# Kernel tuning notes

Measured on AMD Instinct MI355X. Metric: run time of the kernel, lower is better.

The kernel has to match this reference:

```python
import jax, jax.numpy as jnp
import numpy as np

NPOINT = 2048
RADII = (0.4, 0.8)
NSAMPLES = (16, 32)
EPS = 1e-5


def _fps(xyz, npoint):
    # iterative farthest point sampling, start at index 0 (matches CUDA kernel)
    B, N, _ = xyz.shape

    def step(carry, _):
        dist, last = carry  # dist [B,N], last [B]
        lx = jnp.take_along_axis(xyz, last[:, None, None], axis=1)  # [B,1,3]
        d = jnp.sum((xyz - lx) ** 2, axis=-1)  # [B,N]
        dist = jnp.minimum(dist, d)
        nxt = jnp.argmax(dist, axis=1).astype(jnp.int32)
        return (dist, nxt), last

    init = (jnp.full((B, N), 1e10, xyz.dtype), jnp.zeros((B,), jnp.int32))
    _, idxs = jax.lax.scan(step, init, None, length=npoint)
    return idxs.T  # [B, npoint]


def _ball_query(radius, nsample, xyz, new_xyz):
    # first-nsample points within radius, in original order; pad with first hit (0 if none)
    N = xyz.shape[1]
    d2 = jnp.sum((new_xyz[:, :, None, :] - xyz[:, None, :, :]) ** 2, axis=-1)  # [B,S,N]
    mask = d2 < radius * radius
    ar = jnp.arange(N, dtype=jnp.int32)
    key = jnp.where(mask, ar, N + ar)  # in-range first, stable original order
    order = jnp.argsort(key, axis=-1)[..., :nsample].astype(jnp.int32)  # [B,S,ns]
    cnt = mask.sum(axis=-1, keepdims=True)  # [B,S,1]
    valid = jnp.arange(nsample) < cnt
    return jnp.where(valid, order, order[..., :1])


def _bn_relu(x):
    # training-mode BatchNorm (gamma=1, beta=0) over all dims but channel (last)
    red = tuple(range(x.ndim - 1))
    mu = x.mean(axis=red, keepdims=True)
    var = x.var(axis=red, keepdims=True)
    return jax.nn.relu((x - mu) * jax.lax.rsqrt(var + EPS))


def _scale(xyz, new_xyz, feats, radius, nsample, ws):
    idx = _ball_query(radius, nsample, xyz, new_xyz)  # [B,S,ns]
    B, S, ns = idx.shape
    flat = idx.reshape(B, S * ns)
    gx = jnp.take_along_axis(xyz, flat[..., None], axis=1).reshape(B, S, ns, 3)
    gx = gx - new_xyz[:, :, None, :]  # relative coords
    gf = jnp.take_along_axis(feats, flat[..., None], axis=1).reshape(B, S, ns, -1)
    h = jnp.concatenate([gx, gf], axis=-1)  # [B,S,ns,3+C]
    for w in ws:
        h = _bn_relu(h @ w)  # pointwise conv (kernel 1) + BN + ReLU
    return h.max(axis=2)  # max-pool over group -> [B,S,Cout]


def setup_inputs() -> dict:
    key = jax.random.key(0)
    ks = jax.random.split(key, 16)
    s = 0.02
    return {
        "xyz": jax.random.normal(ks[0], (8, 8192, 3), jnp.float32),
        "features": jax.random.normal(ks[1], (8, 8192, 64), jnp.float32),
        "w0_0": jax.random.normal(ks[2], (67, 64), jnp.float32) * s,
        "w0_1": jax.random.normal(ks[3], (64, 64), jnp.float32) * s,
        "w0_2": jax.random.normal(ks[4], (64, 128), jnp.float32) * s,
        "w1_0": jax.random.normal(ks[5], (67, 64), jnp.float32) * s,
        "w1_1": jax.random.normal(ks[6], (64, 64), jnp.float32) * s,
        "w1_2": jax.random.normal(ks[7], (64, 128), jnp.float32) * s,
        "agg_w": jax.random.normal(ks[8], (256, 256), jnp.float32) * s,
        "agg_b": jax.random.normal(ks[9], (256,), jnp.float32) * s,
        "conf_w": jax.random.normal(ks[10], (256, 256), jnp.float32) * s,
        "cls_w": jax.random.normal(ks[11], (256, 3), jnp.float32) * s,
        "cls_b": jax.random.normal(ks[12], (3,), jnp.float32) * s,
    }


def reference(xyz, features, w0_0, w0_1, w0_2, w1_0, w1_1, w1_2,
              agg_w, agg_b, conf_w, cls_w, cls_b):
    idx = _fps(xyz, NPOINT)  # [B,S]
    new_xyz = jnp.take_along_axis(xyz, idx[..., None], axis=1)  # [B,S,3]
    f0 = _scale(xyz, new_xyz, features, RADII[0], NSAMPLES[0], (w0_0, w0_1, w0_2))
    f1 = _scale(xyz, new_xyz, features, RADII[1], NSAMPLES[1], (w1_0, w1_1, w1_2))
    h = jnp.concatenate([f0, f1], axis=-1)  # [B,S,256]
    h = _bn_relu(h @ agg_w + agg_b)  # aggregation Linear + BN + ReLU
    c = _bn_relu(h @ conf_w)  # confidence hidden layer
    cls = c @ cls_w + cls_b  # [B,S,num_class]
    return new_xyz, h, cls
```

## Files before the change

kernel.cpp:

```cpp
#include <hip/hip_runtime.h>
#include <cstdint>
#include <cstddef>

constexpr int Bb = 8;
constexpr int Nn = 8192;
constexpr int Ss = 2048;
constexpr int BS = Bb * Ss;
constexpr int NSL = 32;

typedef float vfloat2 __attribute__((ext_vector_type(2)));

__global__ __launch_bounds__(1024) void fps_kernel(const float* __restrict__ xyz,
                                                   float* __restrict__ new_xyz) {
  __shared__ float lx[Nn * 3];
  __shared__ int sidx[Ss];
  __shared__ unsigned long long slotV[2];
  __shared__ int slotI[2];
  const int b = blockIdx.x;
  const int tid = threadIdx.x;
  const float* xb = xyz + (size_t)b * Nn * 3;
  for (int e = tid; e < Nn * 3; e += 1024) lx[e] = xb[e];
  if (tid == 0) {
    slotV[0] = 0ull; slotV[1] = 0ull;
    slotI[0] = 0x7fffffff; slotI[1] = 0x7fffffff;
  }
  __syncthreads();

  vfloat2 px2[4], py2[4], pz2[4], df2[4];
  double dist[8];
#pragma unroll
  for (int jj = 0; jj < 4; ++jj) {
    const int p0 = tid + (2 * jj) * 1024, p1 = tid + (2 * jj + 1) * 1024;
    px2[jj] = (vfloat2){lx[p0 * 3 + 0], lx[p1 * 3 + 0]};
    py2[jj] = (vfloat2){lx[p0 * 3 + 1], lx[p1 * 3 + 1]};
    pz2[jj] = (vfloat2){lx[p0 * 3 + 2], lx[p1 * 3 + 2]};
    df2[jj] = (vfloat2){3.0e38f, 3.0e38f};
    dist[2 * jj] = 1e10;
    dist[2 * jj + 1] = 1e10;
  }
  float lmax = 3.0e38f;
  int cur = 0;
  double lv = -1.0;
  int li = 0x7fffffff;
  float lv32 = -1.0f;
  float wv32_c = -1.0f;
  for (int i = 0; i < Ss; ++i) {
    if (tid == 0) sidx[i] = cur;
    const float cxf = lx[cur * 3 + 0], cyf = lx[cur * 3 + 1], czf = lx[cur * 3 + 2];
    const vfloat2 cx2 = {cxf, cxf}, cy2 = {cyf, cyf}, cz2 = {czf, czf};
    const bool wasTop = (lv32 == wv32_c);
    vfloat2 d2v[4];
#pragma unroll
    for (int jj = 0; jj < 4; ++jj) {
      const vfloat2 dx = px2[jj] - cx2;
      const vfloat2 dy = py2[jj] - cy2;
      const vfloat2 dz = pz2[jj] - cz2;
      d2v[jj] = dx * dx + dy * dy + dz * dz;
    }
    const float dmin = fminf(fminf(fminf(d2v[0].x, d2v[0].y), fminf(d2v[1].x, d2v[1].y)),
                             fminf(fminf(d2v[2].x, d2v[2].y), fminf(d2v[3].x, d2v[3].y)));
    bool changed = false;
    if (dmin <= lmax) {
#pragma unroll
      for (int j = 0; j < 8; ++j) {
        const float d2s = d2v[j >> 1][j & 1];
        const float dfs = (j & 1) ? df2[j >> 1].y : df2[j >> 1].x;
        if (d2s <= dfs) {
          const float pxs = px2[j >> 1][j & 1];
          const float pys = py2[j >> 1][j & 1];
          const float pzs = pz2[j >> 1][j & 1];
          double dx = __dsub_rn((double)pxs, (double)cxf);
          double dy = __dsub_rn((double)pys, (double)cyf);
          double dz = __dsub_rn((double)pzs, (double)czf);
          double d = __dadd_rn(__dadd_rn(__dmul_rn(dx, dx), __dmul_rn(dy, dy)),
                               __dmul_rn(dz, dz));
          if (d < dist[j]) {
            dist[j] = d;
            const float dfn = (float)d * 1.000002f;
            if (j & 1) df2[j >> 1].y = dfn; else df2[j >> 1].x = dfn;
            changed = true;
          }
        }
      }
      if (changed) {
        lv = -1.0;
        li = 0;
#pragma unroll
        for (int j = 0; j < 8; ++j) {
          if (dist[j] > lv) { lv = dist[j]; li = tid + j * 1024; }
        }
        lv32 = (float)lv;
        lmax = fmaxf(fmaxf(fmaxf(df2[0].x, df2[0].y), fmaxf(df2[1].x, df2[1].y)),
                     fmaxf(fmaxf(df2[2].x, df2[2].y), fmaxf(df2[3].x, df2[3].y)));
      }
    }
    const unsigned long long topChanged = __ballot(changed && wasTop);
    if (topChanged) {
      float m32 = lv32;
#pragma unroll
      for (int off = 1; off < 64; off <<= 1) m32 = fmaxf(m32, __shfl_xor(m32, off));
      wv32_c = m32;
    }
    const int pb = i & 1;
    if (lv32 == wv32_c) atomicMax(&slotV[pb], (unsigned long long)__double_as_longlong(lv));
    __syncthreads();
    const double W = __longlong_as_double((long long)slotV[pb]);
    if (lv == W) atomicMin(&slotI[pb], li);
    if (tid == 0) {
      slotV[pb ^ 1] = 0ull;
      slotI[pb ^ 1] = 0x7fffffff;
    }
    __syncthreads();
    cur = slotI[pb];
  }
  __syncthreads();
  float* nxb = new_xyz + (size_t)b * Ss * 3;
  for (int e = tid; e < Ss * 3; e += 1024) {
    const int i = e / 3, c = e - i * 3;
    nxb[e] = lx[sidx[i] * 3 + c];
  }
}

__global__ __launch_bounds__(256) void ballq_kernel(const float* __restrict__ xyz,
                                                    const float* __restrict__ nxyz,
                                                    int* __restrict__ idx0,
                                                    int* __restrict__ idx1) {
  const int wid = threadIdx.x >> 6, lane = threadIdx.x & 63;
  const int bs = blockIdx.x * 4 + wid;
  const int b = bs >> 11;
  const float* xb = xyz + (size_t)b * Nn * 3;
  const float cxf = nxyz[bs * 3 + 0];
  const float cyf = nxyz[bs * 3 + 1];
  const float czf = nxyz[bs * 3 + 2];
  const double R0d = 0.4 * 0.4, R1d = 0.8 * 0.8;
  const float R0lo = 0.16f * (1.0f - 1e-5f), R0hi = 0.16f * (1.0f + 1e-5f);
  const float R1lo = 0.64f * (1.0f - 1e-5f), R1hi = 0.64f * (1.0f + 1e-5f);
  int cnt0 = 0, cnt1 = 0, first0 = 0, first1 = 0;
  const unsigned long long lmask = (1ull << lane) - 1ull;
  for (int base = 0; base < Nn; base += 64) {
    const int p = base + lane;
    const float pxs = xb[p * 3 + 0], pys = xb[p * 3 + 1], pzs = xb[p * 3 + 2];
    const float dxf = pxs - cxf, dyf = pys - cyf, dzf = pzs - czf;
    const float d2f = fmaf(dxf, dxf, fmaf(dyf, dyf, dzf * dzf));
    bool in0, in1;
    if (d2f < R0lo) in0 = true;
    else if (d2f > R0hi) in0 = false;
    else {
      double dx = __dsub_rn((double)pxs, (double)cxf);
      double dy = __dsub_rn((double)pys, (double)cyf);
      double dz = __dsub_rn((double)pzs, (double)czf);
      double d2 = __dadd_rn(__dadd_rn(__dmul_rn(dx, dx), __dmul_rn(dy, dy)), __dmul_rn(dz, dz));
      in0 = d2 < R0d;
    }
    if (d2f < R1lo) in1 = true;
    else if (d2f > R1hi) in1 = false;
    else {
      double dx = __dsub_rn((double)pxs, (double)cxf);
      double dy = __dsub_rn((double)pys, (double)cyf);
      double dz = __dsub_rn((double)pzs, (double)czf);
      double d2 = __dadd_rn(__dadd_rn(__dmul_rn(dx, dx), __dmul_rn(dy, dy)), __dmul_rn(dz, dz));
      in1 = d2 < R1d;
    }
    unsigned long long m0 = __ballot(in0);
    unsigned long long m1 = __ballot(in1);
    if (cnt0 < 16 && m0) {
      if (cnt0 == 0) first0 = base + __builtin_ctzll(m0);
      int r = (int)__popcll(m0 & lmask);
      if (in0 && cnt0 + r < 16) idx0[bs * 16 + cnt0 + r] = p;
      cnt0 += (int)__popcll(m0);
    }
    if (cnt1 < 32 && m1) {
      if (cnt1 == 0) first1 = base + __builtin_ctzll(m1);
      int r = (int)__popcll(m1 & lmask);
      if (in1 && cnt1 + r < 32) idx1[bs * 32 + cnt1 + r] = p;
      cnt1 += (int)__popcll(m1);
    }
    if (cnt0 >= 16 && cnt1 >= 32) break;
  }
  const int f0 = cnt0 < 16 ? cnt0 : 16;
  for (int j = f0 + lane; j < 16; j += 64) idx0[bs * 16 + j] = first0;
  const int f1 = cnt1 < 32 ? cnt1 : 32;
  for (int j = f1 + lane; j < 32; j += 64) idx1[bs * 32 + j] = first1;
}

template <int COUT, int KTOT, int MODE, int NS, bool POOL, bool BIAS>
__global__ __launch_bounds__(256) void mlp_gemm(
    const float* __restrict__ xin, const float* __restrict__ xin2,
    const float* __restrict__ stIn, const float* __restrict__ stIn2,
    float invM1, float invM2,
    const float* __restrict__ w, const float* __restrict__ bias,
    const int* __restrict__ gidx, const float* __restrict__ xyz,
    const float* __restrict__ nxyz, const float* __restrict__ feats,
    float* __restrict__ hw, float* __restrict__ out, float* __restrict__ Sout) {
  constexpr int KC = (KTOT <= 68) ? KTOT : 32;
  constexpr int NCH = (KTOT + KC - 1) / KC;
  constexpr int TC = COUT / 16;
  constexpr int TC2 = TC / 2;
  constexpr int XPAD = KC + 1;
  constexpr int XSZ = 64 * XPAD;
  constexpr int EPI = (POOL ? 48 : 32) * COUT;
  constexpr int SM = (XSZ + KC * COUT > EPI) ? (XSZ + KC * COUT) : EPI;
  constexpr int BNSZ = (MODE == 0) ? 0 : 512;
  __shared__ float smem[SM + BNSZ];
  __shared__ int rowP[(MODE == 0) ? 64 : 1];
  __shared__ float rowC[(MODE == 0) ? 192 : 1];
  float* xS = smem;
  float* wS = smem + XSZ;
  float* bnM = smem + SM;
  float* bnR = smem + SM + 256;

  const int tid = threadIdx.x;
  const int cg = tid & 15, rg = tid >> 4;
  const int row0 = blockIdx.x * 64;

  if constexpr (MODE == 0) {
    if (tid < 64) {
      const int rowg = row0 + tid;
      const int bs = rowg / NS;
      const int bb = bs >> 11;
      rowP[tid] = bb * Nn + gidx[rowg];
      rowC[tid * 3 + 0] = nxyz[bs * 3 + 0];
      rowC[tid * 3 + 1] = nxyz[bs * 3 + 1];
      rowC[tid * 3 + 2] = nxyz[bs * 3 + 2];
    }
    __syncthreads();
  } else {
    for (int c = tid; c < KTOT; c += 256) {
      float sum = 0.f, sq = 0.f, im;
      if constexpr (MODE == 2) {
        const float* base = (c < 128) ? stIn : stIn2;
        const int cc = (c < 128) ? c : c - 128;
        im = (c < 128) ? invM1 : invM2;
#pragma unroll
        for (int s = 0; s < NSL; ++s) {
          sum += base[cc * NSL + s];
          sq += base[(128 + cc) * NSL + s];
        }
      } else {
        constexpr int C = (MODE == 1) ? 64 : 256;
        im = invM1;
#pragma unroll
        for (int s = 0; s < NSL; ++s) {
          sum += stIn[c * NSL + s];
          sq += stIn[(C + c) * NSL + s];
        }
      }
      const float mu = sum * im;
      const float var = sq * im - mu * mu;
      bnM[c] = mu;
      bnR[c] = 1.0f / sqrtf(var + 1e-5f);
    }
    __syncthreads();
  }

  vfloat2 acc2[4][TC2];
#pragma unroll
  for (int i = 0; i < 4; ++i)
#pragma unroll
    for (int t = 0; t < TC2; ++t) acc2[i][t] = (vfloat2){0.f, 0.f};

  for (int ch = 0; ch < NCH; ++ch) {
    const int k0 = ch * KC;
    if (ch) __syncthreads();
    for (int e = tid; e < 64 * KC; e += 256) {
      const int r = e / KC, kk = e - r * KC;
      const int kg = k0 + kk;
      const int rowg = row0 + r;
      float v;
      if constexpr (MODE == 0) {
        if (kg < 3)
          v = xyz[rowP[r] * 3 + kg] - rowC[r * 3 + kg];
        else
          v = feats[(rowP[r] << 6) + (kg - 3)];
      } else if constexpr (MODE == 1) {
        v = fmaxf((xin[(size_t)rowg * 64 + kg] - bnM[kg]) * bnR[kg], 0.f);
      } else if constexpr (MODE == 2) {
        if (kg < 128)
          v = fmaxf((xin[(size_t)rowg * 128 + kg] - bnM[kg]) * bnR[kg], 0.f);
        else
          v = fmaxf((xin2[(size_t)rowg * 128 + (kg - 128)] - bnM[kg]) * bnR[kg], 0.f);
      } else {
        v = fmaxf((xin[(size_t)rowg * 256 + kg] - bnM[kg]) * bnR[kg], 0.f);
        hw[(size_t)rowg * 256 + kg] = v;
      }
      xS[r * XPAD + kk] = v;
    }
    for (int e = tid; e < KC * COUT; e += 256) {
      const int kk = e / COUT, c = e - kk * COUT;
      wS[kk * COUT + c] = w[(size_t)(k0 + kk) * COUT + c];
    }
    __syncthreads();
    for (int kk = 0; kk < KC; ++kk) {
      vfloat2 x2[4];
#pragma unroll
      for (int i = 0; i < 4; ++i) {
        const float xr = xS[(rg * 4 + i) * XPAD + kk];
        x2[i] = (vfloat2){xr, xr};
      }
#pragma unroll
      for (int t2 = 0; t2 < TC2; t2 += 2) {
        const float4 wv = *(const float4*)&wS[kk * COUT + cg * TC + 2 * t2];
        const vfloat2 w0 = {wv.x, wv.y}, w1 = {wv.z, wv.w};
#pragma unroll
        for (int i = 0; i < 4; ++i) {
          acc2[i][t2] += x2[i] * w0;
          acc2[i][t2 + 1] += x2[i] * w1;
        }
      }
    }
  }
  __syncthreads();
  if constexpr (BIAS) {
#pragma unroll
    for (int t = 0; t < TC; ++t) {
      const float bv = bias[cg * TC + t];
#pragma unroll
      for (int i = 0; i < 4; ++i) {
        if (t & 1) acc2[i][t >> 1].y += bv; else acc2[i][t >> 1].x += bv;
      }
    }
  }
  float* ssum = smem;
  float* ssq = smem + 16 * COUT;
  float* pbuf = smem + 32 * COUT;
  const int colb = cg * TC;
#pragma unroll
  for (int t = 0; t < TC; ++t) {
    float s = 0.f, q = 0.f, m = -3.4e38f;
#pragma unroll
    for (int i = 0; i < 4; ++i) {
      const float v = (t & 1) ? acc2[i][t >> 1].y : acc2[i][t >> 1].x;
      s += v;
      q = fmaf(v, v, q);
      m = fmaxf(m, v);
    }
    ssum[rg * COUT + colb + t] = s;
    ssq[rg * COUT + colb + t] = q;
    if constexpr (POOL) pbuf[rg * COUT + colb + t] = m;
  }
  __syncthreads();
  const int slot = blockIdx.x & (NSL - 1);
  for (int c = tid; c < COUT; c += 256) {
    float s = 0.f, q = 0.f;
#pragma unroll
    for (int rr = 0; rr < 16; ++rr) {
      s += ssum[rr * COUT + c];
      q += ssq[rr * COUT + c];
    }
    atomicAdd(&Sout[c * NSL + slot], s);
    atomicAdd(&Sout[(COUT + c) * NSL + slot], q);
  }
  if constexpr (POOL) {
    constexpr int G = 64 / NS, RPG = NS / 4;
    for (int o = tid; o < G * COUT; o += 256) {
      const int g = o / COUT, c = o - g * COUT;
      float m = pbuf[(g * RPG) * COUT + c];
#pragma unroll
      for (int qq = 1; qq < RPG; ++qq) m = fmaxf(m, pbuf[(g * RPG + qq) * COUT + c]);
      out[(size_t)(blockIdx.x * G + g) * COUT + c] = m;
    }
  } else {
#pragma unroll
    for (int i = 0; i < 4; ++i) {
      float* op = out + (size_t)(row0 + rg * 4 + i) * COUT + colb;
#pragma unroll
      for (int t2 = 0; t2 < TC2; t2 += 2) {
        *(float4*)(op + 2 * t2) = make_float4(acc2[i][t2].x, acc2[i][t2].y,
                                              acc2[i][t2 + 1].x, acc2[i][t2 + 1].y);
      }
    }
  }
}

__global__ __launch_bounds__(256) void cls_kernel(const float* __restrict__ craw,
                                                  const float* __restrict__ st,
                                                  const float* __restrict__ clsw,
                                                  const float* __restrict__ clsb,
                                                  float* __restrict__ outc) {
  __shared__ float bnM[256], bnR[256];
  const int tid = threadIdx.x;
  {
    float sum = 0.f, sq = 0.f;
#pragma unroll
    for (int s = 0; s < NSL; ++s) {
      sum += st[tid * NSL + s];
      sq += st[(256 + tid) * NSL + s];
    }
    const float im = 1.0f / 16384.0f;
    const float mu = sum * im;
    const float var = sq * im - mu * mu;
    bnM[tid] = mu;
    bnR[tid] = 1.0f / sqrtf(var + 1e-5f);
  }
  __syncthreads();
  const int wid = tid >> 6, lane = tid & 63;
  const int row = blockIdx.x * 4 + wid;
  const float* cr = craw + (size_t)row * 256;
  float a0 = 0.f, a1 = 0.f, a2 = 0.f;
#pragma unroll 4
  for (int k = lane; k < 256; k += 64) {
    float x = fmaxf((cr[k] - bnM[k]) * bnR[k], 0.f);
    a0 = fmaf(x, clsw[k * 3 + 0], a0);
    a1 = fmaf(x, clsw[k * 3 + 1], a1);
    a2 = fmaf(x, clsw[k * 3 + 2], a2);
  }
#pragma unroll
  for (int off = 32; off; off >>= 1) {
    a0 += __shfl_down(a0, off);
    a1 += __shfl_down(a1, off);
    a2 += __shfl_down(a2, off);
  }
  if (lane == 0) {
    outc[row * 3 + 0] = a0 + clsb[0];
    outc[row * 3 + 1] = a1 + clsb[1];
    outc[row * 3 + 2] = a2 + clsb[2];
  }
}

extern "C" void kernel_launch(void* const* d_in, const int* in_sizes, int n_in,
                              void* d_out, int out_size, void* d_ws, size_t ws_size,
                              hipStream_t stream) {
  (void)in_sizes; (void)n_in; (void)out_size; (void)ws_size;
  const float* xyz = (const float*)d_in[0];
  const float* feats = (const float*)d_in[1];
  const float* w00 = (const float*)d_in[2];
  const float* w01 = (const float*)d_in[3];
  const float* w02 = (const float*)d_in[4];
  const float* w10 = (const float*)d_in[5];
  const float* w11 = (const float*)d_in[6];
  const float* w12 = (const float*)d_in[7];
  const float* aggw = (const float*)d_in[8];
  const float* aggb = (const float*)d_in[9];
  const float* confw = (const float*)d_in[10];
  const float* clsw = (const float*)d_in[11];
  const float* clsb = (const float*)d_in[12];

  float* outp = (float*)d_out;
  float* nxyz = outp;
  float* hout = outp + (size_t)BS * 3;
  float* clsout = hout + (size_t)BS * 256;

  char* ws = (char*)d_ws;
  const size_t MB = 1u << 20;
  int* idx0 = (int*)(ws + 0);
  int* idx1 = (int*)(ws + 1 * MB);
  float* st = (float*)(ws + 3 * MB);
  float* pool0 = (float*)(ws + 12 * MB);
  float* pool1 = (float*)(ws + 20 * MB);
  float* aggraw = (float*)(ws + 28 * MB);
  float* confraw = (float*)(ws + 44 * MB);
  float* hA = (float*)(ws + 60 * MB);

  hipMemsetAsync(st, 0, 65536 * sizeof(float), stream);

  const float iM0 = 1.0f / 262144.0f;
  const float iM1 = 1.0f / 524288.0f;
  const float iMh = 1.0f / 16384.0f;

  fps_kernel<<<Bb, 1024, 0, stream>>>(xyz, nxyz);
  ballq_kernel<<<BS / 4, 256, 0, stream>>>(xyz, nxyz, idx0, idx1);

  mlp_gemm<64, 67, 0, 16, false, false><<<4096, 256, 0, stream>>>(
      nullptr, nullptr, nullptr, nullptr, 0.f, 0.f, w00, nullptr,
      idx0, xyz, nxyz, feats, nullptr, hA, st + 0);
  mlp_gemm<64, 64, 1, 1, false, false><<<4096, 256, 0, stream>>>(
      hA, nullptr, st + 0, nullptr, iM0, 0.f, w01, nullptr,
      nullptr, nullptr, nullptr, nullptr, nullptr, hA, st + 4096);
  mlp_gemm<128, 64, 1, 16, true, false><<<4096, 256, 0, stream>>>(
      hA, nullptr, st + 4096, nullptr, iM0, 0.f, w02, nullptr,
      nullptr, nullptr, nullptr, nullptr, nullptr, pool0, st + 8192);

  mlp_gemm<64, 67, 0, 32, false, false><<<8192, 256, 0, stream>>>(
      nullptr, nullptr, nullptr, nullptr, 0.f, 0.f, w10, nullptr,
      idx1, xyz, nxyz, feats, nullptr, hA, st + 16384);
  mlp_gemm<64, 64, 1, 1, false, false><<<8192, 256, 0, stream>>>(
      hA, nullptr, st + 16384, nullptr, iM1, 0.f, w11, nullptr,
      nullptr, nullptr, nullptr, nullptr, nullptr, hA, st + 20480);
  mlp_gemm<128, 64, 1, 32, true, false><<<8192, 256, 0, stream>>>(
      hA, nullptr, st + 20480, nullptr, iM1, 0.f, w12, nullptr,
      nullptr, nullptr, nullptr, nullptr, nullptr, pool1, st + 24576);

  mlp_gemm<256, 256, 2, 1, false, true><<<256, 256, 0, stream>>>(
      pool0, pool1, st + 8192, st + 24576, iM0, iM1, aggw, aggb,
      nullptr, nullptr, nullptr, nullptr, nullptr, aggraw, st + 32768);

  mlp_gemm<256, 256, 4, 1, false, false><<<256, 256, 0, stream>>>(
      aggraw, nullptr, st + 32768, nullptr, iMh, 0.f, confw, nullptr,
      nullptr, nullptr, nullptr, nullptr, hout, confraw, st + 49152);

  cls_kernel<<<BS / 4, 256, 0, stream>>>(confraw, st + 49152, clsw, clsb, clsout);
}
```

Measured before the change: 3.679 ms.

## Replace FPS shared-memory atomics with per-wave argmax and cross-wave shuffle reduction

Swaps the two-phase atomicMax/atomicMin argmax in farthest point sampling for a cached per-wave (value, index) winner in double precision. The winner is recomputed by shuffles only when the top lane changed, written per wave to a double-buffered shared array, and reduced across the 16 waves by every wave with shuffles. This removes one __syncthreads per iteration and the shared atomics. In exchange each wave does a redundant 16-entry reduction with 64-bit shuffles, and the cached per-wave reduction uses doubles instead of floats.

Result: slower. 4.714 ms (+28.1%).

```diff
diff --git a/kernel.cpp b/kernel.cpp
--- a/kernel.cpp
+++ b/kernel.cpp
@@ -14,16 +14,13 @@
                                                    float* __restrict__ new_xyz) {
   __shared__ float lx[Nn * 3];
   __shared__ int sidx[Ss];
-  __shared__ unsigned long long slotV[2];
-  __shared__ int slotI[2];
+  __shared__ double sVal[2][16];
+  __shared__ int sIdxW[2][16];
   const int b = blockIdx.x;
   const int tid = threadIdx.x;
+  const int wid = tid >> 6, lane = tid & 63;
   const float* xb = xyz + (size_t)b * Nn * 3;
   for (int e = tid; e < Nn * 3; e += 1024) lx[e] = xb[e];
-  if (tid == 0) {
-    slotV[0] = 0ull; slotV[1] = 0ull;
-    slotI[0] = 0x7fffffff; slotI[1] = 0x7fffffff;
-  }
   __syncthreads();
 
   vfloat2 px2[4], py2[4], pz2[4], df2[4];
@@ -42,13 +39,13 @@
   int cur = 0;
   double lv = -1.0;
   int li = 0x7fffffff;
-  float lv32 = -1.0f;
-  float wv32_c = -1.0f;
+  double wVal = -1.0;
+  int wIdx = 0x7fffffff;
   for (int i = 0; i < Ss; ++i) {
     if (tid == 0) sidx[i] = cur;
     const float cxf = lx[cur * 3 + 0], cyf = lx[cur * 3 + 1], czf = lx[cur * 3 + 2];
     const vfloat2 cx2 = {cxf, cxf}, cy2 = {cyf, cyf}, cz2 = {czf, czf};
-    const bool wasTop = (lv32 == wv32_c);
+    const bool wasTop = (lv == wVal);
     vfloat2 d2v[4];
 #pragma unroll
     for (int jj = 0; jj < 4; ++jj) {
@@ -89,29 +86,37 @@
         for (int j = 0; j < 8; ++j) {
           if (dist[j] > lv) { lv = dist[j]; li = tid + j * 1024; }
         }
-        lv32 = (float)lv;
         lmax = fmaxf(fmaxf(fmaxf(df2[0].x, df2[0].y), fmaxf(df2[1].x, df2[1].y)),
                      fmaxf(fmaxf(df2[2].x, df2[2].y), fmaxf(df2[3].x, df2[3].y)));
       }
     }
-    const unsigned long long topChanged = __ballot(changed && wasTop);
-    if (topChanged) {
-      float m32 = lv32;
-#pragma unroll
-      for (int off = 1; off < 64; off <<= 1) m32 = fmaxf(m32, __shfl_xor(m32, off));
-      wv32_c = m32;
+    if (__any(changed && wasTop)) {
+      double v = lv;
+      int ii = li;
+#pragma unroll
+      for (int off = 1; off < 64; off <<= 1) {
+        const double ov = __shfl_xor(v, off);
+        const int oi = __shfl_xor(ii, off);
+        if (ov > v || (ov == v && oi < ii)) { v = ov; ii = oi; }
+      }
+      wVal = v;
+      wIdx = ii;
     }
     const int pb = i & 1;
-    if (lv32 == wv32_c) atomicMax(&slotV[pb], (unsigned long long)__double_as_longlong(lv));
+    if (lane == 0) {
+      sVal[pb][wid] = wVal;
+      sIdxW[pb][wid] = wIdx;
+    }
     __syncthreads();
-    const double W = __longlong_as_double((long long)slotV[pb]);
-    if (lv == W) atomicMin(&slotI[pb], li);
-    if (tid == 0) {
-      slotV[pb ^ 1] = 0ull;
-      slotI[pb ^ 1] = 0x7fffffff;
-    }
-    __syncthreads();
-    cur = slotI[pb];
+    double bv = sVal[pb][lane & 15];
+    int bi = sIdxW[pb][lane & 15];
+#pragma unroll
+    for (int off = 1; off < 16; off <<= 1) {
+      const double ov = __shfl_xor(bv, off);
+      const int oi = __shfl_xor(bi, off);
+      if (ov > bv || (ov == bv && oi < bi)) { bv = ov; bi = oi; }
+    }
+    cur = bi;
   }
   __syncthreads();
   float* nxb = new_xyz + (size_t)b * Ss * 3;
```

## Run pointwise MLP GEMMs on MFMA using split-bf16 three-product emulation

Applied to the files above, without the earlier changes.

Replaces the scalar FP32 register-tiled GEMM in mlp_gemm with bf16 MFMA 16x16x32 instructions. Each operand is split into high and low bf16 parts, and three products are accumulated to approximate FP32 precision. K is padded to a multiple of 32, weights are stored transposed in LDS, and the epilogue is remapped to the MFMA output layout. The GEMM FLOPs move onto matrix cores, at the cost of extra conversion work and an approximation of full FP32 accuracy. The total time likely includes FPS and ball query, which this change leaves untouched.

Result: no change. 3.725 ms (+1.3%).

```diff
diff --git a/kernel.cpp b/kernel.cpp
--- a/kernel.cpp
+++ b/kernel.cpp
@@ -9,6 +9,13 @@
 constexpr int NSL = 32;
 
 typedef float vfloat2 __attribute__((ext_vector_type(2)));
+typedef short bf16x8 __attribute__((ext_vector_type(8)));
+typedef float f32x4 __attribute__((ext_vector_type(4)));
+
+__device__ __forceinline__ unsigned short f32_to_bf16(float f) {
+  unsigned u = __float_as_uint(f);
+  return (unsigned short)((u + 0x7FFFu + ((u >> 16) & 1u)) >> 16);
+}
 
 __global__ __launch_bounds__(1024) void fps_kernel(const float* __restrict__ xyz,
                                                    float* __restrict__ new_xyz) {
@@ -192,25 +199,31 @@
     const int* __restrict__ gidx, const float* __restrict__ xyz,
     const float* __restrict__ nxyz, const float* __restrict__ feats,
     float* __restrict__ hw, float* __restrict__ out, float* __restrict__ Sout) {
-  constexpr int KC = (KTOT <= 68) ? KTOT : 32;
-  constexpr int NCH = (KTOT + KC - 1) / KC;
-  constexpr int TC = COUT / 16;
-  constexpr int TC2 = TC / 2;
-  constexpr int XPAD = KC + 1;
-  constexpr int XSZ = 64 * XPAD;
-  constexpr int EPI = (POOL ? 48 : 32) * COUT;
-  constexpr int SM = (XSZ + KC * COUT > EPI) ? (XSZ + KC * COUT) : EPI;
-  constexpr int BNSZ = (MODE == 0) ? 0 : 512;
-  __shared__ float smem[SM + BNSZ];
+  constexpr int KP = (KTOT + 31) & ~31;
+  constexpr int KC = (KP <= 96) ? KP : 64;
+  constexpr int NCH = KP / KC;
+  constexpr int CT = COUT / 16;
+  constexpr int XPus = KC + 8;
+  constexpr int XPL = 64 * XPus;
+  constexpr int WPL = COUT * XPus;
+  constexpr size_t STAGE_B = (size_t)(2 * XPL + 2 * WPL) * 2;
+  constexpr size_t EPI_B = (size_t)(POOL ? 48 : 32) * COUT * 4;
+  constexpr size_t BODY_B = (STAGE_B > EPI_B) ? STAGE_B : EPI_B;
+  constexpr size_t BN_B = (MODE == 0) ? 0 : 2048;
+  __shared__ __align__(16) unsigned char smraw[BODY_B + BN_B];
   __shared__ int rowP[(MODE == 0) ? 64 : 1];
   __shared__ float rowC[(MODE == 0) ? 192 : 1];
-  float* xS = smem;
-  float* wS = smem + XSZ;
-  float* bnM = smem + SM;
-  float* bnR = smem + SM + 256;
+  unsigned short* xH = (unsigned short*)smraw;
+  unsigned short* xL = xH + XPL;
+  unsigned short* wH = xL + XPL;
+  unsigned short* wL = wH + WPL;
+  float* bnM = (float*)(smraw + BODY_B);
+  float* bnR = bnM + 256;
 
   const int tid = threadIdx.x;
-  const int cg = tid & 15, rg = tid >> 4;
+  const int l15 = tid & 15;
+  const int lq = (tid >> 4) & 3;
+  const int wv = tid >> 6;
   const int row0 = blockIdx.x * 64;
 
   if constexpr (MODE == 0) {
@@ -253,11 +266,9 @@
     __syncthreads();
   }
 
-  vfloat2 acc2[4][TC2];
-#pragma unroll
-  for (int i = 0; i < 4; ++i)
-#pragma unroll
-    for (int t = 0; t < TC2; ++t) acc2[i][t] = (vfloat2){0.f, 0.f};
+  f32x4 acc[CT];
+#pragma unroll
+  for (int t = 0; t < CT; ++t) acc[t] = (f32x4){0.f, 0.f, 0.f, 0.f};
 
   for (int ch = 0; ch < NCH; ++ch) {
     const int k0 = ch * KC;
@@ -267,7 +278,9 @@
       const int kg = k0 + kk;
       const int rowg = row0 + r;
       float v;
-      if constexpr (MODE == 0) {
+      if (kg >= KTOT) {
+        v = 0.f;
+      } else if constexpr (MODE == 0) {
         if (kg < 3)
           v = xyz[rowP[r] * 3 + kg] - rowC[r * 3 + kg];
         else
@@ -283,63 +296,71 @@
         v = fmaxf((xin[(size_t)rowg * 256 + kg] - bnM[kg]) * bnR[kg], 0.f);
         hw[(size_t)rowg * 256 + kg] = v;
       }
-      xS[r * XPAD + kk] = v;
+      const unsigned short hb = f32_to_bf16(v);
+      const float vhf = __uint_as_float(((unsigned)hb) << 16);
+      const unsigned short lb = f32_to_bf16(v - vhf);
+      xH[r * XPus + kk] = hb;
+      xL[r * XPus + kk] = lb;
     }
     for (int e = tid; e < KC * COUT; e += 256) {
       const int kk = e / COUT, c = e - kk * COUT;
-      wS[kk * COUT + c] = w[(size_t)(k0 + kk) * COUT + c];
+      const int kg = k0 + kk;
+      const float wvv = (kg < KTOT) ? w[(size_t)kg * COUT + c] : 0.f;
+      const unsigned short hb = f32_to_bf16(wvv);
+      const float vhf = __uint_as_float(((unsigned)hb) << 16);
+      const unsigned short lb = f32_to_bf16(wvv - vhf);
+      wH[c * XPus + kk] = hb;
+      wL[c * XPus + kk] = lb;
     }
     __syncthreads();
-    for (int kk = 0; kk < KC; ++kk) {
-      vfloat2 x2[4];
-#pragma unroll
-      for (int i = 0; i < 4; ++i) {
-        const float xr = xS[(rg * 4 + i) * XPAD + kk];
-        x2[i] = (vfloat2){xr, xr};
-      }
-#pragma unroll
-      for (int t2 = 0; t2 < TC2; t2 += 2) {
-        const float4 wv = *(const float4*)&wS[kk * COUT + cg * TC + 2 * t2];
-        const vfloat2 w0 = {wv.x, wv.y}, w1 = {wv.z, wv.w};
-#pragma unroll
-        for (int i = 0; i < 4; ++i) {
-          acc2[i][t2] += x2[i] * w0;
-          acc2[i][t2 + 1] += x2[i] * w1;
-        }
+    const unsigned short* axh = xH + (16 * wv + l15) * XPus + lq * 8;
+    const unsigned short* axl = xL + (16 * wv + l15) * XPus + lq * 8;
+#pragma unroll
+    for (int kb = 0; kb < KC; kb += 32) {
+      const bf16x8 ah = *(const bf16x8*)(axh + kb);
+      const bf16x8 al = *(const bf16x8*)(axl + kb);
+#pragma unroll
+      for (int ct = 0; ct < CT; ++ct) {
+        const unsigned short* bwh = wH + (ct * 16 + l15) * XPus + lq * 8 + kb;
+        const unsigned short* bwl = wL + (ct * 16 + l15) * XPus + lq * 8 + kb;
+        const bf16x8 bh = *(const bf16x8*)bwh;
+        const bf16x8 bl = *(const bf16x8*)bwl;
+        acc[ct] = __builtin_amdgcn_mfma_f32_16x16x32_bf16(al, bh, acc[ct], 0, 0, 0);
+        acc[ct] = __builtin_amdgcn_mfma_f32_16x16x32_bf16(ah, bl, acc[ct], 0, 0, 0);
+        acc[ct] = __builtin_amdgcn_mfma_f32_16x16x32_bf16(ah, bh, acc[ct], 0, 0, 0);
       }
     }
   }
   __syncthreads();
   if constexpr (BIAS) {
 #pragma unroll
-    for (int t = 0; t < TC; ++t) {
-      const float bv = bias[cg * TC + t];
-#pragma unroll
-      for (int i = 0; i < 4; ++i) {
-        if (t & 1) acc2[i][t >> 1].y += bv; else acc2[i][t >> 1].x += bv;
-      }
-    }
-  }
-  float* ssum = smem;
-  float* ssq = smem + 16 * COUT;
-  float* pbuf = smem + 32 * COUT;
-  const int colb = cg * TC;
-#pragma unroll
-  for (int t = 0; t < TC; ++t) {
+    for (int ct = 0; ct < CT; ++ct) {
+      const float bv = bias[ct * 16 + l15];
+#pragma unroll
+      for (int r = 0; r < 4; ++r) acc[ct][r] += bv;
+    }
+  }
+  float* ssum = (float*)smraw;
+  float* ssq = ssum + 16 * COUT;
+  float* pbuf = ssq + 16 * COUT;
+  const int slot = tid >> 4;
+#pragma unroll
+  for (int ct = 0; ct < CT; ++ct) {
+    const int col = ct * 16 + l15;
     float s = 0.f, q = 0.f, m = -3.4e38f;
 #pragma unroll
-    for (int i = 0; i < 4; ++i) {
-      const float v = (t & 1) ? acc2[i][t >> 1].y : acc2[i][t >> 1].x;
+    for (int r = 0; r < 4; ++r) {
+      const float v = acc[ct][r];
       s += v;
       q = fmaf(v, v, q);
       m = fmaxf(m, v);
     }
-    ssum[rg * COUT + colb + t] = s;
-    ssq[rg * COUT + colb + t] = q;
-    if constexpr (POOL) pbuf[rg * COUT + colb + t] = m;
+    ssum[slot * COUT + col] = s;
+    ssq[slot * COUT + col] = q;
+    if constexpr (POOL) pbuf[slot * COUT + col] = m;
   }
   __syncthreads();
-  const int slot = blockIdx.x & (NSL - 1);
+  const int aslot = blockIdx.x & (NSL - 1);
   for (int c = tid; c < COUT; c += 256) {
     float s = 0.f, q = 0.f;
 #pragma unroll
@@ -347,26 +368,25 @@
       s += ssum[rr * COUT + c];
       q += ssq[rr * COUT + c];
     }
-    atomicAdd(&Sout[c * NSL + slot], s);
-    atomicAdd(&Sout[(COUT + c) * NSL + slot], q);
+    atomicAdd(&Sout[c * NSL + aslot], s);
+    atomicAdd(&Sout[(COUT + c) * NSL + aslot], q);
   }
   if constexpr (POOL) {
-    constexpr int G = 64 / NS, RPG = NS / 4;
+    constexpr int G = 64 / NS;
+    constexpr int SPG = 16 / G;
     for (int o = tid; o < G * COUT; o += 256) {
       const int g = o / COUT, c = o - g * COUT;
-      float m = pbuf[(g * RPG) * COUT + c];
-#pragma unroll
-      for (int qq = 1; qq < RPG; ++qq) m = fmaxf(m, pbuf[(g * RPG + qq) * COUT + c]);
+      float m = pbuf[(g * SPG) * COUT + c];
+#pragma unroll
+      for (int s = 1; s < SPG; ++s) m = fmaxf(m, pbuf[(g * SPG + s) * COUT + c]);
       out[(size_t)(blockIdx.x * G + g) * COUT + c] = m;
     }
   } else {
 #pragma unroll
-    for (int i = 0; i < 4; ++i) {
-      float* op = out + (size_t)(row0 + rg * 4 + i) * COUT + colb;
-#pragma unroll
-      for (int t2 = 0; t2 < TC2; t2 += 2) {
-        *(float4*)(op + 2 * t2) = make_float4(acc2[i][t2].x, acc2[i][t2].y,
-                                              acc2[i][t2 + 1].x, acc2[i][t2 + 1].y);
+    for (int ct = 0; ct < CT; ++ct) {
+#pragma unroll
+      for (int r = 0; r < 4; ++r) {
+        out[(size_t)(row0 + 16 * wv + lq * 4 + r) * COUT + ct * 16 + l15] = acc[ct][r];
       }
     }
   }
```
